# Performance work log

Measured on AMD Instinct MI355X. Metric: run time of the kernel, lower is better.

The kernel has to match this reference:

```python
import jax, jax.numpy as jnp
from jax import lax
import numpy as np

# pywt.Wavelet('sym5').dec_lo; true convolution with rec_lo == correlation with dec_lo
_DEC_LO = jnp.array([0.027333068345077982, 0.029519490925774643, -0.039134249302383094,
                     0.1993975339773936, 0.7234076904024206, 0.6339789634582119,
                     0.01660210576452232, -0.17532808990845047, -0.021101834024758855,
                     0.019538882735286728], dtype=jnp.float32)
_KERNEL = _DEC_LO[None, None, :]  # (O=1, I=1, L=10)


def _idwt_approx(c):
    # One inverse-DWT level with zero detail coeffs.
    # pywt idwt: upsample by 2, full conv with rec_lo, slice [L-2 : L-2 + 2n-L+2].
    # Equivalent: lhs_dilation=2, padding=(1,1), correlation with dec_lo.
    B, n = c.shape
    out = lax.conv_general_dilated(c[:, None, :], _KERNEL, window_strides=(1,),
                                   padding=[(1, 1)], lhs_dilation=(2,),
                                   dimension_numbers=('NCH', 'OIH', 'NCH'))
    return out[:, 0, :]  # (B, 2n - 8)


def _waverec3(cA):
    # waverec with coeffs [cA(20), zeros(20), zeros(31), zeros(54)], sym5 -> length 100
    a = _idwt_approx(cA)      # 20 -> 32
    a = a[:, :31]             # pywt waverec crops a to len(d)=31
    a = _idwt_approx(a)       # 31 -> 54
    a = _idwt_approx(a)       # 54 -> 100
    return a


def _ce(logits, target):
    logp = jax.nn.log_softmax(logits, axis=-1)
    return -jnp.take_along_axis(logp, target[:, None], axis=-1)[:, 0]


def _ohem(logits, target, train_mask, ratio=3.0):
    ce = _ce(logits, target)
    tf = target.astype(jnp.float32)
    pos = (tf * train_mask) > 0
    neg = ((1.0 - tf) * train_mask) > 0
    n_pos = jnp.sum(pos.astype(jnp.float32))
    count_neg = jnp.sum(neg.astype(jnp.float32))
    loss_pos = jnp.where(n_pos > 0, jnp.sum(jnp.where(pos, ce, 0.0)), 0.0)
    n_neg = jnp.where(n_pos > 0, jnp.minimum(count_neg, jnp.floor(ratio * n_pos)), 100.0)
    srt = jnp.sort(jnp.where(neg, ce, -jnp.inf))[::-1]
    take = (jnp.arange(srt.shape[0]) < n_neg) & jnp.isfinite(srt)
    loss_neg = jnp.sum(jnp.where(take, srt, 0.0))
    return (loss_pos + loss_neg) / (n_pos + n_neg)


def _smooth_l1(d):
    ad = jnp.abs(d)
    return jnp.where(ad < 1.0, 0.5 * d * d, ad - 0.5)


def _forward_single(cls_pred, reg_pred, gt):
    cp = jnp.transpose(cls_pred, (0, 2, 3, 1)).reshape(-1, 4)
    rp = jnp.transpose(reg_pred, (0, 2, 3, 1)).reshape(-1, 42)
    g = jnp.transpose(gt, (0, 2, 3, 1)).reshape(-1, 45)
    tr_pred, tcl_pred = cp[:, :2], cp[:, 2:]
    wl_r, xc_p, wl_i, yc_p = rp[:, :20], rp[:, 20], rp[:, 21:41], rp[:, 41]
    tr_mask, tcl_mask, train_mask = g[:, 0], g[:, 1], g[:, 2]
    real_g, xc_g, imag_g, yc_g = g[:, 3:23], g[:, 23], g[:, 24:44], g[:, 44]
    ttm = train_mask * tr_mask
    n_pos = jnp.sum(ttm)

    loss_tr = _ohem(tr_pred, tr_mask.astype(jnp.int32), train_mask)

    ce_tcl = _ce(tcl_pred, tcl_mask.astype(jnp.int32))
    neg_m = 1.0 - ttm
    mp = jnp.sum(ce_tcl * ttm) / jnp.maximum(n_pos, 1.0)
    mn = jnp.sum(ce_tcl * neg_m) / jnp.maximum(jnp.sum(neg_m), 1.0)
    loss_tcl = jnp.where(n_pos > 0, mp + 0.5 * mn, 0.0)

    px = _waverec3(wl_r) + xc_p[:, None]   # (M,100)
    py = _waverec3(wl_i) + yc_p[:, None]
    gx = _waverec3(real_g) + xc_g[:, None]
    gy = _waverec3(imag_g) + yc_g[:, None]
    per_pix = jnp.sum(_smooth_l1(px - gx) + _smooth_l1(py - gy), axis=-1)  # (M,)
    loss_contour = jnp.where(n_pos > 0, 0.5 * jnp.sum(ttm * per_pix) / (n_pos * 200.0), 0.0)
    return jnp.stack([loss_tr, loss_tcl, loss_contour])


def setup_inputs() -> dict:
    key = jax.random.key(0)
    N = 8
    out = {}
    for name, H in (("3", 100), ("4", 50), ("5", 25)):
        k1, k2, k3, k4, k5, k6 = jax.random.split(jax.random.fold_in(key, int(name)), 6)
        out["cls" + name] = jax.random.normal(k1, (N, 4, H, H), jnp.float32)
        out["reg" + name] = jax.random.normal(k2, (N, 42, H, H), jnp.float32)
        tr = jax.random.bernoulli(k3, 0.1, (N, 1, H, H)).astype(jnp.float32)
        tcl = jax.random.bernoulli(k4, 0.5, (N, 1, H, H)).astype(jnp.float32)
        train = jax.random.bernoulli(k5, 0.9, (N, 1, H, H)).astype(jnp.float32)
        rest = jax.random.normal(k6, (N, 42, H, H), jnp.float32)
        out["gt" + name] = jnp.concatenate([tr, tcl, train, rest], axis=1)  # 45 ch
    return out


def reference(cls3, reg3, gt3, cls4, reg4, gt4, cls5, reg5, gt5):
    total = (_forward_single(cls3, reg3, gt3)
             + _forward_single(cls4, reg4, gt4)
             + _forward_single(cls5, reg5, gt5))
    return total  # [loss_text, loss_center, loss_contour]
```

## Files before the change

kernel.cpp:

```cpp
#include <hip/hip_runtime.h>
#include <math.h>

#define DEVI __device__ __forceinline__

static constexpr float KD[10] = {
  0.027333068345077982f,  0.029519490925774643f, -0.039134249302383094f,
  0.1993975339773936f,    0.7234076904024206f,    0.6339789634582119f,
  0.01660210576452232f,  -0.17532808990845047f,  -0.021101834024758855f,
  0.019538882735286728f};

#define CE_OFF     0
#define PH_OFF     105056
#define PH1_REL    40192
#define PH2_REL    50432
#define MH_OFF     160608
#define BS_OFF     234336
#define SLOTGT_OFF 308064
#define STATE_OFF  308352
#define SLOT2_OFF  308384
#define CBUF_OFF   308672
#define CAPC       49152
#define PART_OFF   456128
#define PART_STRIDE 3840

#define NB3 157
#define NB4 40
#define NB5 20
#define NBR 96

DEVI float wave_sum(float v) {
#pragma unroll
  for (int d = 32; d; d >>= 1) v += __shfl_down(v, d);
  return v;
}

DEVI float block_sum(float v, float* sh) {
  int lane = threadIdx.x & 63, wid = threadIdx.x >> 6;
  v = wave_sum(v);
  if (lane == 0) sh[wid] = v;
  __syncthreads();
  if (threadIdx.x == 0) {
    float s = 0.f;
    int nw = blockDim.x >> 6;
    for (int w = 0; w < nw; ++w) s += sh[w];
    sh[0] = s;
  }
  __syncthreads();
  float r = sh[0];
  __syncthreads();
  return r;
}

DEVI int suffix_scan_256(int v, int* sh) {
  int t = threadIdx.x;
  sh[t] = v;
  __syncthreads();
#pragma unroll
  for (int off = 1; off < 256; off <<= 1) {
    int x = (t + off < 256) ? sh[t + off] : 0;
    __syncthreads();
    sh[t] += x;
    __syncthreads();
  }
  return sh[t];
}

DEVI float sl1(float v) { float a = fabsf(v); return (a < 1.f) ? 0.5f * v * v : a - 0.5f; }

DEVI float ce2cls(float la, float lb, float tgt) {
  float m = fmaxf(la, lb);
  float lse = m + __logf(__expf(la - m) + __expf(lb - m));
  return lse - ((tgt > 0.5f) ? lb : la);
}

DEVI float recon_full(const float* __restrict__ rb, const float* __restrict__ gb,
                      int rc0, int gc0, size_t HW, float off) {
  float c[20];
#pragma unroll
  for (int i = 0; i < 20; ++i)
    c[i] = rb[(size_t)(rc0 + i) * HW] - gb[(size_t)(gc0 + i) * HW];
  float a1w0=0.f,a1w1=0.f,a1w2=0.f,a1w3=0.f,a1w4=0.f;
  float a2w0=0.f,a2w1=0.f,a2w2=0.f,a2w3=0.f,a2w4=0.f;
  float acc = 0.f;
#pragma unroll
  for (int j1 = 0; j1 < 31; ++j1) {
    int b = j1 >> 1;
    float a1v;
    if (j1 & 1)
      a1v = KD[0]*c[b] + KD[2]*c[b+1] + KD[4]*c[b+2] + KD[6]*c[b+3] + KD[8]*c[b+4];
    else
      a1v = KD[1]*c[b] + KD[3]*c[b+1] + KD[5]*c[b+2] + KD[7]*c[b+3] + KD[9]*c[b+4];
    a1w0=a1w1; a1w1=a1w2; a1w2=a1w3; a1w3=a1w4; a1w4=a1v;
    if (j1 >= 4) {
#pragma unroll
      for (int tt = 0; tt < 2; ++tt) {
        float a2v;
        if (tt)
          a2v = KD[0]*a1w0 + KD[2]*a1w1 + KD[4]*a1w2 + KD[6]*a1w3 + KD[8]*a1w4;
        else
          a2v = KD[1]*a1w0 + KD[3]*a1w1 + KD[5]*a1w2 + KD[7]*a1w3 + KD[9]*a1w4;
        a2w0=a2w1; a2w1=a2w2; a2w2=a2w3; a2w3=a2w4; a2w4=a2v;
        int j2 = 2 * (j1 - 4) + tt;
        if (j2 >= 4) {
          acc += sl1(KD[1]*a2w0 + KD[3]*a2w1 + KD[5]*a2w2 + KD[7]*a2w3 + KD[9]*a2w4 + off);
          acc += sl1(KD[0]*a2w0 + KD[2]*a2w1 + KD[4]*a2w2 + KD[6]*a2w3 + KD[8]*a2w4 + off);
        }
      }
    }
  }
  return acc;
}

DEVI float2 recon2_full(const float* __restrict__ rb, const float* __restrict__ gb,
                        int rc0, int gc0, size_t HW, float2 off) {
  float2 c[20];
#pragma unroll
  for (int i = 0; i < 20; ++i) {
    float2 rv = *(const float2*)(rb + (size_t)(rc0 + i) * HW);
    float2 gv = *(const float2*)(gb + (size_t)(gc0 + i) * HW);
    c[i].x = rv.x - gv.x; c[i].y = rv.y - gv.y;
  }
  float2 a1w0={0,0},a1w1={0,0},a1w2={0,0},a1w3={0,0},a1w4={0,0};
  float2 a2w0={0,0},a2w1={0,0},a2w2={0,0},a2w3={0,0},a2w4={0,0};
  float2 acc={0,0};
#pragma unroll
  for (int j1 = 0; j1 < 31; ++j1) {
    int b = j1 >> 1;
    float2 a1v;
    if (j1 & 1) {
      a1v.x = KD[0]*c[b].x + KD[2]*c[b+1].x + KD[4]*c[b+2].x + KD[6]*c[b+3].x + KD[8]*c[b+4].x;
      a1v.y = KD[0]*c[b].y + KD[2]*c[b+1].y + KD[4]*c[b+2].y + KD[6]*c[b+3].y + KD[8]*c[b+4].y;
    } else {
      a1v.x = KD[1]*c[b].x + KD[3]*c[b+1].x + KD[5]*c[b+2].x + KD[7]*c[b+3].x + KD[9]*c[b+4].x;
      a1v.y = KD[1]*c[b].y + KD[3]*c[b+1].y + KD[5]*c[b+2].y + KD[7]*c[b+3].y + KD[9]*c[b+4].y;
    }
    a1w0=a1w1; a1w1=a1w2; a1w2=a1w3; a1w3=a1w4; a1w4=a1v;
    if (j1 >= 4) {
#pragma unroll
      for (int tt = 0; tt < 2; ++tt) {
        float2 a2v;
        if (tt) {
          a2v.x = KD[0]*a1w0.x + KD[2]*a1w1.x + KD[4]*a1w2.x + KD[6]*a1w3.x + KD[8]*a1w4.x;
          a2v.y = KD[0]*a1w0.y + KD[2]*a1w1.y + KD[4]*a1w2.y + KD[6]*a1w3.y + KD[8]*a1w4.y;
        } else {
          a2v.x = KD[1]*a1w0.x + KD[3]*a1w1.x + KD[5]*a1w2.x + KD[7]*a1w3.x + KD[9]*a1w4.x;
          a2v.y = KD[1]*a1w0.y + KD[3]*a1w1.y + KD[5]*a1w2.y + KD[7]*a1w3.y + KD[9]*a1w4.y;
        }
        a2w0=a2w1; a2w1=a2w2; a2w2=a2w3; a2w3=a2w4; a2w4=a2v;
        int j2 = 2 * (j1 - 4) + tt;
        if (j2 >= 4) {
          float vex = KD[1]*a2w0.x + KD[3]*a2w1.x + KD[5]*a2w2.x + KD[7]*a2w3.x + KD[9]*a2w4.x + off.x;
          float vey = KD[1]*a2w0.y + KD[3]*a2w1.y + KD[5]*a2w2.y + KD[7]*a2w3.y + KD[9]*a2w4.y + off.y;
          float vox = KD[0]*a2w0.x + KD[2]*a2w1.x + KD[4]*a2w2.x + KD[6]*a2w3.x + KD[8]*a2w4.x + off.x;
          float voy = KD[0]*a2w0.y + KD[2]*a2w1.y + KD[4]*a2w2.y + KD[6]*a2w3.y + KD[8]*a2w4.y + off.y;
          acc.x += sl1(vex) + sl1(vox);
          acc.y += sl1(vey) + sl1(voy);
        }
      }
    }
  }
  return acc;
}

__global__ void __launch_bounds__(256, 2)
pixel_kernel(const float* __restrict__ cls3, const float* __restrict__ reg3, const float* __restrict__ gt3,
             const float* __restrict__ cls4, const float* __restrict__ reg4, const float* __restrict__ gt4,
             const float* __restrict__ cls5, const float* __restrict__ reg5, const float* __restrict__ gt5,
             float* __restrict__ ws, float* __restrict__ out) {
  int bx = blockIdx.x, axis = blockIdx.y, t = threadIdx.x;
  const float *cls, *reg, *gt;
  int M, HW, ceOff, partBase, phRel, nb, lbx, two;
  if (bx < NB3) {
    cls = cls3; reg = reg3; gt = gt3; M = 80000; HW = 10000;
    ceOff = 0; partBase = PART_OFF; phRel = 0; nb = NB3; lbx = bx; two = 1;
  } else if (bx < NB3 + NB4) {
    cls = cls4; reg = reg4; gt = gt4; M = 20000; HW = 2500;
    ceOff = 80000; partBase = PART_OFF + PART_STRIDE; phRel = PH1_REL; nb = NB4; lbx = bx - NB3; two = 1;
  } else {
    cls = cls5; reg = reg5; gt = gt5; M = 5000; HW = 625;
    ceOff = 100000; partBase = PART_OFF + 2 * PART_STRIDE; phRel = PH2_REL; nb = NB5; lbx = bx - NB3 - NB4; two = 0;
  }
  float* ceArr = ws + ceOff;
  unsigned* ph = (unsigned*)(ws + PH_OFF) + phRel;

  if (bx == 0 && axis == 0 && t < 3) out[t] = 0.f;

  __shared__ unsigned hlds[256];
  __shared__ float shp[4][6];
  hlds[t] = 0u;
  __syncthreads();

  float cnt_pos = 0.f, cnt_neg = 0.f, s_ce_pos = 0.f, s_tcl_ttm = 0.f, s_tcl_negm = 0.f;
  float s_ttm_pp = 0.f;
  int rc0 = axis ? 21 : 0;
  int gc0 = axis ? 24 : 3;

  if (two) {
    int p0 = (lbx * 256 + t) * 2;
    if (p0 < M) {
      int n = p0 / HW, hw = p0 % HW;
      const float* gb = gt  + (size_t)n * 45 * HW + hw;
      const float* rb = reg + (size_t)n * 42 * HW + hw;
      float2 trv = *(const float2*)(gb);
      float2 tnv = *(const float2*)(gb + 2 * (size_t)HW);
      float2 ttm; ttm.x = trv.x * tnv.x; ttm.y = trv.y * tnv.y;

      if (axis == 0) {
        const float* cb = cls + (size_t)n * 4 * HW + hw;
        float2 l0 = *(const float2*)(cb);
        float2 l1 = *(const float2*)(cb + (size_t)HW);
        float2 l2 = *(const float2*)(cb + 2 * (size_t)HW);
        float2 l3 = *(const float2*)(cb + 3 * (size_t)HW);
        float2 tcl = *(const float2*)(gb + (size_t)HW);
        float cex = ce2cls(l0.x, l1.x, trv.x), cey = ce2cls(l0.y, l1.y, trv.y);
        float ctx = ce2cls(l2.x, l3.x, tcl.x), cty = ce2cls(l2.y, l3.y, tcl.y);
        bool posx = ttm.x > 0.f, posy = ttm.y > 0.f;
        bool negx = ((1.f - trv.x) * tnv.x) > 0.f, negy = ((1.f - trv.y) * tnv.y) > 0.f;
        float cvx = negx ? cex : 0.f, cvy = negy ? cey : 0.f;
        float2 cev; cev.x = cvx; cev.y = cvy;
        *(float2*)(ceArr + p0) = cev;
        if (negx) atomicAdd(&hlds[__float_as_uint(cvx) >> 23], 1u);
        if (negy) atomicAdd(&hlds[__float_as_uint(cvy) >> 23], 1u);
        cnt_pos = (posx ? 1.f : 0.f) + (posy ? 1.f : 0.f);
        cnt_neg = (negx ? 1.f : 0.f) + (negy ? 1.f : 0.f);
        s_ce_pos = (posx ? cex : 0.f) + (posy ? cey : 0.f);
        s_tcl_ttm = ctx * ttm.x + cty * ttm.y;
        s_tcl_negm = ctx * (1.f - ttm.x) + cty * (1.f - ttm.y);
      }

      float2 rcv = *(const float2*)(rb + (size_t)(rc0 + 20) * HW);
      float2 gcv = *(const float2*)(gb + (size_t)(gc0 + 20) * HW);
      float2 dc; dc.x = rcv.x - gcv.x; dc.y = rcv.y - gcv.y;
      float2 pp = recon2_full(rb, gb, rc0, gc0, (size_t)HW, dc);
      s_ttm_pp = ttm.x * pp.x + ttm.y * pp.y;
    }
  } else {
    int p = lbx * 256 + t;
    if (p < M) {
      int n = p / HW, hw = p % HW;
      const float* gb = gt  + (size_t)n * 45 * HW + hw;
      const float* rb = reg + (size_t)n * 42 * HW + hw;
      float tr = gb[0], train = gb[2 * (size_t)HW];
      float ttm = tr * train;
      if (axis == 0) {
        const float* cb = cls + (size_t)n * 4 * HW + hw;
        float ce_tr = ce2cls(cb[0], cb[(size_t)HW], tr);
        float ce_tcl = ce2cls(cb[2 * (size_t)HW], cb[3 * (size_t)HW], gb[(size_t)HW]);
        bool pos = ttm > 0.f;
        bool neg = ((1.f - tr) * train) > 0.f;
        float cev = neg ? ce_tr : 0.f;
        ceArr[p] = cev;
        if (neg) atomicAdd(&hlds[__float_as_uint(cev) >> 23], 1u);
        cnt_pos = pos ? 1.f : 0.f;
        cnt_neg = neg ? 1.f : 0.f;
        s_ce_pos = pos ? ce_tr : 0.f;
        s_tcl_ttm = ce_tcl * ttm;
        s_tcl_negm = ce_tcl * (1.f - ttm);
      }
      float dc = rb[(size_t)(rc0 + 20) * HW] - gb[(size_t)(gc0 + 20) * HW];
      float pp = recon_full(rb, gb, rc0, gc0, (size_t)HW, dc);
      s_ttm_pp = ttm * pp;
    }
  }

  int lane = t & 63, wid = t >> 6;
  cnt_pos = wave_sum(cnt_pos);
  cnt_neg = wave_sum(cnt_neg);
  s_ce_pos = wave_sum(s_ce_pos);
  s_tcl_ttm = wave_sum(s_tcl_ttm);
  s_tcl_negm = wave_sum(s_tcl_negm);
  s_ttm_pp = wave_sum(s_ttm_pp);
  if (lane == 0) {
    shp[wid][0] = cnt_pos; shp[wid][1] = cnt_neg; shp[wid][2] = s_ce_pos;
    shp[wid][3] = s_tcl_ttm; shp[wid][4] = s_tcl_negm; shp[wid][5] = s_ttm_pp;
  }
  __syncthreads();
  if (t < 6) {
    float s = shp[0][t] + shp[1][t] + shp[2][t] + shp[3][t];
    ws[partBase + (size_t)(axis * nb + lbx) * 6 + t] = s;
  }
  if (axis == 0)
    ph[(size_t)lbx * 256 + t] = hlds[t];
}

__global__ void refine_kernel(float* __restrict__ ws) {
  int s = blockIdx.y, r = blockIdx.x, t = threadIdx.x;
  int M   = (s == 0) ? 80000 : (s == 1 ? 20000 : 5000);
  int off = (s == 0) ? 0     : (s == 1 ? 80000 : 100000);
  int nb0 = (s == 0) ? NB3   : (s == 1 ? NB4   : NB5);
  int phRel = (s == 0) ? 0 : (s == 1 ? PH1_REL : PH2_REL);
  int* st = (int*)(ws + STATE_OFF) + s * 8;

  __shared__ int sh[256];
  __shared__ int sel[2];
  __shared__ float red[4];
  __shared__ unsigned hW[4][256];
  __shared__ unsigned mhL[256];
  __shared__ float bsL[256];

  const float* part = ws + PART_OFF + s * PART_STRIDE;
  int npart = 2 * nb0;
  float a0 = 0.f, a1 = 0.f, a2 = 0.f, a3 = 0.f, a4 = 0.f, a5 = 0.f;
  for (int i = t; i < npart; i += 256) {
    const float* p6 = part + (size_t)i * 6;
    a0 += p6[0]; a1 += p6[1]; a2 += p6[2]; a3 += p6[3]; a4 += p6[4]; a5 += p6[5];
  }
  a0 = block_sum(a0, red);
  a1 = block_sum(a1, red);
  a2 = block_sum(a2, red);
  a3 = block_sum(a3, red);
  a4 = block_sum(a4, red);
  a5 = block_sum(a5, red);

  float cnt_pos = a0, cnt_negf = a1;
  int cnt_neg = (int)cnt_negf;
  float kf = (cnt_pos > 0.f) ? fminf(cnt_negf, floorf(3.f * cnt_pos)) : 100.f;
  int k_take = min((int)kf, cnt_neg);

  int ibin, rem;
  if (k_take >= cnt_neg) { ibin = -1; rem = 0; }
  else if (k_take <= 0)  { ibin = 256; rem = 0; }
  else {
    const uint4* ph4 = (const uint4*)((const unsigned*)(ws + PH_OFF) + phRel);
    unsigned c0 = 0u, c1 = 0u, c2 = 0u, c3 = 0u;
    int n4 = nb0 * 64;
    for (int i = t; i < n4; i += 256) {
      uint4 u = ph4[i];
      c0 += u.x; c1 += u.y; c2 += u.z; c3 += u.w;
    }
    int wid = t >> 6, b0 = (4 * t) & 255;
    hW[wid][b0 + 0] = c0; hW[wid][b0 + 1] = c1; hW[wid][b0 + 2] = c2; hW[wid][b0 + 3] = c3;
    __syncthreads();
    int h = (int)(hW[0][t] + hW[1][t] + hW[2][t] + hW[3][t]);
    int suf = suffix_scan_256(h, sh);
    int above = suf - h;
    if (suf >= k_take && above < k_take) { sel[0] = t; sel[1] = k_take - above; }
    __syncthreads();
    ibin = sel[0]; rem = sel[1];
    __syncthreads();
  }
  if (r == 0 && t == 0) {
    st[0] = ibin; st[1] = rem;
    float* stf = (float*)st;
    stf[2] = kf; stf[3] = a0; stf[4] = a2; stf[5] = a3; stf[6] = a4; stf[7] = a5;
  }

  mhL[t] = 0u; bsL[t] = 0.f;
  __syncthreads();
  const float* ce = ws + off;
  float sum = 0.f;
  for (int i = r * 256 + t; i < M; i += NBR * 256) {
    float v = ce[i];
    unsigned b = __float_as_uint(v);
    int e = (int)(b >> 23);
    if (e > ibin) sum += v;
    else if (e == ibin && rem > 0) {
      int m8 = (int)((b >> 15) & 255u);
      atomicAdd(&mhL[m8], 1u);
      atomicAdd(&bsL[m8], v);
    }
  }
  sum = block_sum(sum, red);
  if (t == 0) ws[SLOTGT_OFF + s * NBR + r] = sum;
  if (rem > 0) {
    ((unsigned*)(ws + MH_OFF))[((size_t)s * NBR + r) * 256 + t] = mhL[t];
    ws[BS_OFF + ((size_t)s * NBR + r) * 256 + t] = bsL[t];
  }
}

__global__ void compactB_kernel(float* __restrict__ ws) {
  int s = blockIdx.y, r = blockIdx.x, t = threadIdx.x;
  int M   = (s == 0) ? 80000 : (s == 1 ? 20000 : 5000);
  int off = (s == 0) ? 0     : (s == 1 ? 80000 : 100000);
  const int* st = (const int*)(ws + STATE_OFF) + s * 8;
  int ibin = st[0], rem = st[1];
  if (rem <= 0) return;

  __shared__ int sh[256];
  __shared__ int sel[2];
  __shared__ float red[4];
  __shared__ unsigned hW[4][256];
  __shared__ unsigned wcnt;

  const unsigned* mh = (const unsigned*)(ws + MH_OFF) + (size_t)s * NBR * 256;
  const uint4* mh4 = (const uint4*)mh;
  unsigned c0 = 0u, c1 = 0u, c2 = 0u, c3 = 0u;
  for (int i = t; i < NBR * 64; i += 256) {
    uint4 u = mh4[i];
    c0 += u.x; c1 += u.y; c2 += u.z; c3 += u.w;
  }
  int wid = t >> 6, b0 = (4 * t) & 255;
  hW[wid][b0 + 0] = c0; hW[wid][b0 + 1] = c1; hW[wid][b0 + 2] = c2; hW[wid][b0 + 3] = c3;
  __syncthreads();
  int h = (int)(hW[0][t] + hW[1][t] + hW[2][t] + hW[3][t]);
  int suf = suffix_scan_256(h, sh);
  int above = suf - h;
  if (suf >= rem && above < rem) { sel[0] = t; }
  __syncthreads();
  int jbin = sel[0];
  __syncthreads();

  float v2 = ws[BS_OFF + ((size_t)s * NBR + r) * 256 + t];
  float gt2 = block_sum((t > jbin) ? v2 : 0.f, red);
  if (t == 0) ws[SLOT2_OFF + s * NBR + r] = gt2;

  int cval = (t < NBR) ? (int)mh[(size_t)t * 256 + jbin] : 0;
  sh[t] = cval;
  __syncthreads();
#pragma unroll
  for (int o = 1; o < 128; o <<= 1) {
    int x = (t >= o) ? sh[t - o] : 0;
    __syncthreads();
    sh[t] += x;
    __syncthreads();
  }
  int base = (r > 0) ? sh[r - 1] : 0;

  if (t == 0) wcnt = 0u;
  __syncthreads();
  const float* ce = ws + off;
  float* cbuf = ws + CBUF_OFF + (size_t)s * CAPC;
  for (int i = r * 256 + t; i < M; i += NBR * 256) {
    float v = ce[i];
    unsigned b = __float_as_uint(v);
    if ((int)(b >> 23) == ibin && (int)((b >> 15) & 255u) == jbin) {
      unsigned idx = (unsigned)base + atomicAdd(&wcnt, 1u);
      if (idx < CAPC) cbuf[idx] = v;
    }
  }
}

__global__ void final_kernel(float* __restrict__ ws, float* __restrict__ out) {
  int s = blockIdx.x, t = threadIdx.x;
  int M = (s == 0) ? 80000 : (s == 1 ? 20000 : 5000);
  const int* st = (const int*)(ws + STATE_OFF) + s * 8;
  const float* stf = (const float*)st;

  __shared__ int sh[256];
  __shared__ int sel[2];
  __shared__ float red[4];
  __shared__ unsigned hW[4][256];
  __shared__ int hist[256];

  int ibin = st[0], rem = st[1];
  float kf = stf[2], n_pos = stf[3];
  float s_ce_pos = stf[4], s_tcl_ttm = stf[5], s_tcl_negm = stf[6], s_ttm_pp = stf[7];

  float lpart = (t < NBR) ? ws[SLOTGT_OFF + s * NBR + t] : 0.f;
  float loss_neg = block_sum(lpart, red);

  if (rem > 0) {
    const uint4* mh4 = (const uint4*)((const unsigned*)(ws + MH_OFF) + (size_t)s * NBR * 256);
    unsigned c0 = 0u, c1 = 0u, c2 = 0u, c3 = 0u;
    for (int i = t; i < NBR * 64; i += 256) {
      uint4 u = mh4[i];
      c0 += u.x; c1 += u.y; c2 += u.z; c3 += u.w;
    }
    int wid = t >> 6, b0 = (4 * t) & 255;
    hW[wid][b0 + 0] = c0; hW[wid][b0 + 1] = c1; hW[wid][b0 + 2] = c2; hW[wid][b0 + 3] = c3;
    __syncthreads();
    int h = (int)(hW[0][t] + hW[1][t] + hW[2][t] + hW[3][t]);
    int suf = suffix_scan_256(h, sh);
    int above = suf - h;
    if (suf >= rem && above < rem) { sel[0] = t; sel[1] = rem - above; }
    __syncthreads();
    int jbin = sel[0], rem2 = sel[1];
    int jcnt = (int)(hW[0][jbin] + hW[1][jbin] + hW[2][jbin] + hW[3][jbin]);
    __syncthreads();

    float l2 = (t < NBR) ? ws[SLOT2_OFF + s * NBR + t] : 0.f;
    loss_neg += block_sum(l2, red);

    int cnt = min(jcnt, CAPC);
    const float* cbuf = ws + CBUF_OFF + (size_t)s * CAPC;

    hist[t] = 0; __syncthreads();
    for (int i = t; i < cnt; i += 256)
      atomicAdd(&hist[(__float_as_uint(cbuf[i]) >> 7) & 255u], 1);
    __syncthreads();
    h = hist[t];
    suf = suffix_scan_256(h, sh);
    above = suf - h;
    int remcur = rem2;
    if (suf >= remcur && above < remcur) { sel[0] = t; sel[1] = remcur - above; }
    __syncthreads();
    int b1 = sel[0]; remcur = sel[1];
    __syncthreads();

    hist[t] = 0; __syncthreads();
    for (int i = t; i < cnt; i += 256) {
      unsigned b = __float_as_uint(cbuf[i]);
      if (((b >> 7) & 255u) == (unsigned)b1) atomicAdd(&hist[b & 127u], 1);
    }
    __syncthreads();
    h = (t < 128) ? hist[t] : 0;
    suf = suffix_scan_256(h, sh);
    above = suf - h;
    if (t < 128 && suf >= remcur && above < remcur) { sel[0] = t; }
    __syncthreads();
    int lb0 = sel[0];
    __syncthreads();

    unsigned prefix = ((unsigned)ibin << 23) | ((unsigned)jbin << 15) |
                      ((unsigned)b1 << 7) | (unsigned)lb0;
    float tval = __uint_as_float(prefix);

    float sum_in = 0.f, cgt = 0.f;
    for (int i = t; i < cnt; i += 256) {
      unsigned b = __float_as_uint(cbuf[i]);
      if (b > prefix) { sum_in += cbuf[i]; cgt += 1.f; }
    }
    sum_in = block_sum(sum_in, red);
    cgt = block_sum(cgt, red);
    loss_neg += sum_in + ((float)rem2 - cgt) * tval;
  }

  if (t == 0) {
    float loss_pos = (n_pos > 0.f) ? s_ce_pos : 0.f;
    float loss_tr = (loss_pos + loss_neg) / (n_pos + kf);

    float negm = (float)M - n_pos;
    float mp = s_tcl_ttm / fmaxf(n_pos, 1.f);
    float mn = s_tcl_negm / fmaxf(negm, 1.f);
    float loss_tcl = (n_pos > 0.f) ? (mp + 0.5f * mn) : 0.f;

    float loss_ct = (n_pos > 0.f) ? (0.5f * s_ttm_pp / (n_pos * 200.f)) : 0.f;

    atomicAdd(&out[0], loss_tr);
    atomicAdd(&out[1], loss_tcl);
    atomicAdd(&out[2], loss_ct);
  }
}

extern "C" void kernel_launch(void* const* d_in, const int* in_sizes, int n_in,
                              void* d_out, int out_size, void* d_ws, size_t ws_size,
                              hipStream_t stream) {
  (void)in_sizes; (void)n_in; (void)out_size; (void)ws_size;
  const float* cls3 = (const float*)d_in[0];
  const float* reg3 = (const float*)d_in[1];
  const float* gt3  = (const float*)d_in[2];
  const float* cls4 = (const float*)d_in[3];
  const float* reg4 = (const float*)d_in[4];
  const float* gt4  = (const float*)d_in[5];
  const float* cls5 = (const float*)d_in[6];
  const float* reg5 = (const float*)d_in[7];
  const float* gt5  = (const float*)d_in[8];

  float* ws = (float*)d_ws;
  float* out = (float*)d_out;

  pixel_kernel<<<dim3(NB3 + NB4 + NB5, 2), 256, 0, stream>>>(
      cls3, reg3, gt3, cls4, reg4, gt4, cls5, reg5, gt5, ws, out);

  refine_kernel<<<dim3(NBR, 3), 256, 0, stream>>>(ws);
  compactB_kernel<<<dim3(NBR, 3), 256, 0, stream>>>(ws);
  final_kernel<<<3, 256, 0, stream>>>(ws, out);
}
```

Measured before the change: 59.42 us.

## Fuse final reduction into compactB via last-block ticket counter

Merges final_kernel into compactB_kernel. Each block takes an atomic ticket after a threadfence, and the last block per scale runs the final selection and loss computation. This removes one kernel launch and its inter-kernel gap. The ticket counter is reset in refine_kernel. The pixel kernel's launch bounds are also raised to 3 blocks per SM for occupancy, which may cause register spilling.

```diff
diff --git a/kernel.cpp b/kernel.cpp
--- a/kernel.cpp
+++ b/kernel.cpp
@@ -22,6 +22,7 @@
 #define CAPC       49152
 #define PART_OFF   456128
 #define PART_STRIDE 3840
+#define TICKET_OFF 467648
 
 #define NB3 157
 #define NB4 40
@@ -162,7 +163,7 @@
   return acc;
 }
 
-__global__ void __launch_bounds__(256, 2)
+__global__ void __launch_bounds__(256, 3)
 pixel_kernel(const float* __restrict__ cls3, const float* __restrict__ reg3, const float* __restrict__ gt3,
              const float* __restrict__ cls4, const float* __restrict__ reg4, const float* __restrict__ gt4,
              const float* __restrict__ cls5, const float* __restrict__ reg5, const float* __restrict__ gt5,
@@ -291,6 +292,8 @@
   int phRel = (s == 0) ? 0 : (s == 1 ? PH1_REL : PH2_REL);
   int* st = (int*)(ws + STATE_OFF) + s * 8;
 
+  if (r == 0 && t == 0) ((unsigned*)(ws + TICKET_OFF))[s] = 0u;
+
   __shared__ int sh[256];
   __shared__ int sel[2];
   __shared__ float red[4];
@@ -368,89 +371,26 @@
   }
 }
 
-__global__ void compactB_kernel(float* __restrict__ ws) {
+__global__ void compactB_kernel(float* __restrict__ ws, float* __restrict__ out) {
   int s = blockIdx.y, r = blockIdx.x, t = threadIdx.x;
   int M   = (s == 0) ? 80000 : (s == 1 ? 20000 : 5000);
   int off = (s == 0) ? 0     : (s == 1 ? 80000 : 100000);
   const int* st = (const int*)(ws + STATE_OFF) + s * 8;
+  const float* stf = (const float*)st;
   int ibin = st[0], rem = st[1];
-  if (rem <= 0) return;
-
-  __shared__ int sh[256];
-  __shared__ int sel[2];
-  __shared__ float red[4];
-  __shared__ unsigned hW[4][256];
-  __shared__ unsigned wcnt;
-
-  const unsigned* mh = (const unsigned*)(ws + MH_OFF) + (size_t)s * NBR * 256;
-  const uint4* mh4 = (const uint4*)mh;
-  unsigned c0 = 0u, c1 = 0u, c2 = 0u, c3 = 0u;
-  for (int i = t; i < NBR * 64; i += 256) {
-    uint4 u = mh4[i];
-    c0 += u.x; c1 += u.y; c2 += u.z; c3 += u.w;
-  }
-  int wid = t >> 6, b0 = (4 * t) & 255;
-  hW[wid][b0 + 0] = c0; hW[wid][b0 + 1] = c1; hW[wid][b0 + 2] = c2; hW[wid][b0 + 3] = c3;
-  __syncthreads();
-  int h = (int)(hW[0][t] + hW[1][t] + hW[2][t] + hW[3][t]);
-  int suf = suffix_scan_256(h, sh);
-  int above = suf - h;
-  if (suf >= rem && above < rem) { sel[0] = t; }
-  __syncthreads();
-  int jbin = sel[0];
-  __syncthreads();
-
-  float v2 = ws[BS_OFF + ((size_t)s * NBR + r) * 256 + t];
-  float gt2 = block_sum((t > jbin) ? v2 : 0.f, red);
-  if (t == 0) ws[SLOT2_OFF + s * NBR + r] = gt2;
-
-  int cval = (t < NBR) ? (int)mh[(size_t)t * 256 + jbin] : 0;
-  sh[t] = cval;
-  __syncthreads();
-#pragma unroll
-  for (int o = 1; o < 128; o <<= 1) {
-    int x = (t >= o) ? sh[t - o] : 0;
-    __syncthreads();
-    sh[t] += x;
-    __syncthreads();
-  }
-  int base = (r > 0) ? sh[r - 1] : 0;
-
-  if (t == 0) wcnt = 0u;
-  __syncthreads();
-  const float* ce = ws + off;
-  float* cbuf = ws + CBUF_OFF + (size_t)s * CAPC;
-  for (int i = r * 256 + t; i < M; i += NBR * 256) {
-    float v = ce[i];
-    unsigned b = __float_as_uint(v);
-    if ((int)(b >> 23) == ibin && (int)((b >> 15) & 255u) == jbin) {
-      unsigned idx = (unsigned)base + atomicAdd(&wcnt, 1u);
-      if (idx < CAPC) cbuf[idx] = v;
-    }
-  }
-}
-
-__global__ void final_kernel(float* __restrict__ ws, float* __restrict__ out) {
-  int s = blockIdx.x, t = threadIdx.x;
-  int M = (s == 0) ? 80000 : (s == 1 ? 20000 : 5000);
-  const int* st = (const int*)(ws + STATE_OFF) + s * 8;
-  const float* stf = (const float*)st;
 
   __shared__ int sh[256];
   __shared__ int sel[2];
   __shared__ float red[4];
   __shared__ unsigned hW[4][256];
   __shared__ int hist[256];
-
-  int ibin = st[0], rem = st[1];
-  float kf = stf[2], n_pos = stf[3];
-  float s_ce_pos = stf[4], s_tcl_ttm = stf[5], s_tcl_negm = stf[6], s_ttm_pp = stf[7];
-
-  float lpart = (t < NBR) ? ws[SLOTGT_OFF + s * NBR + t] : 0.f;
-  float loss_neg = block_sum(lpart, red);
-
+  __shared__ unsigned wcnt;
+  __shared__ unsigned tickL;
+
+  int jbin = 0, rem2 = 0, jcnt = 0;
   if (rem > 0) {
-    const uint4* mh4 = (const uint4*)((const unsigned*)(ws + MH_OFF) + (size_t)s * NBR * 256);
+    const unsigned* mh = (const unsigned*)(ws + MH_OFF) + (size_t)s * NBR * 256;
+    const uint4* mh4 = (const uint4*)mh;
     unsigned c0 = 0u, c1 = 0u, c2 = 0u, c3 = 0u;
     for (int i = t; i < NBR * 64; i += 256) {
       uint4 u = mh4[i];
@@ -464,10 +404,55 @@
     int above = suf - h;
     if (suf >= rem && above < rem) { sel[0] = t; sel[1] = rem - above; }
     __syncthreads();
-    int jbin = sel[0], rem2 = sel[1];
-    int jcnt = (int)(hW[0][jbin] + hW[1][jbin] + hW[2][jbin] + hW[3][jbin]);
-    __syncthreads();
-
+    jbin = sel[0]; rem2 = sel[1];
+    jcnt = (int)(hW[0][jbin] + hW[1][jbin] + hW[2][jbin] + hW[3][jbin]);
+    __syncthreads();
+
+    float v2 = ws[BS_OFF + ((size_t)s * NBR + r) * 256 + t];
+    float gt2 = block_sum((t > jbin) ? v2 : 0.f, red);
+    if (t == 0) ws[SLOT2_OFF + s * NBR + r] = gt2;
+
+    const unsigned* mh_s = mh;
+    int cval = (t < NBR) ? (int)mh_s[(size_t)t * 256 + jbin] : 0;
+    sh[t] = cval;
+    __syncthreads();
+#pragma unroll
+    for (int o = 1; o < 128; o <<= 1) {
+      int x = (t >= o) ? sh[t - o] : 0;
+      __syncthreads();
+      sh[t] += x;
+      __syncthreads();
+    }
+    int base = (r > 0) ? sh[r - 1] : 0;
+
+    if (t == 0) wcnt = 0u;
+    __syncthreads();
+    const float* ce = ws + off;
+    float* cbuf = ws + CBUF_OFF + (size_t)s * CAPC;
+    for (int i = r * 256 + t; i < M; i += NBR * 256) {
+      float v = ce[i];
+      unsigned b = __float_as_uint(v);
+      if ((int)(b >> 23) == ibin && (int)((b >> 15) & 255u) == jbin) {
+        unsigned idx = (unsigned)base + atomicAdd(&wcnt, 1u);
+        if (idx < CAPC) cbuf[idx] = v;
+      }
+    }
+  }
+
+  __threadfence();
+  __syncthreads();
+  if (t == 0) tickL = atomicAdd(&((unsigned*)(ws + TICKET_OFF))[s], 1u);
+  __syncthreads();
+  if (tickL != (unsigned)(NBR - 1)) return;
+  __threadfence();
+
+  float kf = stf[2], n_pos = stf[3];
+  float s_ce_pos = stf[4], s_tcl_ttm = stf[5], s_tcl_negm = stf[6], s_ttm_pp = stf[7];
+
+  float lpart = (t < NBR) ? ws[SLOTGT_OFF + s * NBR + t] : 0.f;
+  float loss_neg = block_sum(lpart, red);
+
+  if (rem > 0 && rem2 > 0) {
     float l2 = (t < NBR) ? ws[SLOT2_OFF + s * NBR + t] : 0.f;
     loss_neg += block_sum(l2, red);
 
@@ -478,9 +463,9 @@
     for (int i = t; i < cnt; i += 256)
       atomicAdd(&hist[(__float_as_uint(cbuf[i]) >> 7) & 255u], 1);
     __syncthreads();
-    h = hist[t];
-    suf = suffix_scan_256(h, sh);
-    above = suf - h;
+    int h = hist[t];
+    int suf = suffix_scan_256(h, sh);
+    int above = suf - h;
     int remcur = rem2;
     if (suf >= remcur && above < remcur) { sel[0] = t; sel[1] = remcur - above; }
     __syncthreads();
@@ -553,6 +538,5 @@
       cls3, reg3, gt3, cls4, reg4, gt4, cls5, reg5, gt5, ws, out);
 
   refine_kernel<<<dim3(NBR, 3), 256, 0, stream>>>(ws);
-  compactB_kernel<<<dim3(NBR, 3), 256, 0, stream>>>(ws);
-  final_kernel<<<3, 256, 0, stream>>>(ws, out);
-}
+  compactB_kernel<<<dim3(NBR, 3), 256, 0, stream>>>(ws, out);
+}
```

Result: slower. 88.37 us (+48.7%).
